# Performance work log

Hardware: AMD Instinct MI355X
Metric: run time of the kernel (lower is better)

Reference implementation:

```python
import jax, jax.numpy as jnp
import numpy as np

N = 100000
E = 1600000
F_IN = 128
F_HID = 64


def setup_inputs() -> dict:
    key = jax.random.key(0)
    ks = jax.random.split(key, 8)
    x = jax.random.normal(ks[0], (N, F_IN), dtype=jnp.float32)
    edge_index = jax.random.randint(ks[1], (2, E), 0, N, dtype=jnp.int64)
    # GCNConv params (PyG default: weight, then bias added after aggregation)
    s1 = 1.0 / np.sqrt(F_IN)
    s2 = 1.0 / np.sqrt(F_HID)
    W1 = jax.random.uniform(ks[2], (F_IN, F_HID), jnp.float32, -s1, s1)
    b1 = jnp.zeros((F_HID,), jnp.float32)
    W2 = jax.random.uniform(ks[3], (F_HID, F_HID), jnp.float32, -s2, s2)
    b2 = jnp.zeros((F_HID,), jnp.float32)
    # Linear(hidden, 1) for predict_link
    Wout = jax.random.uniform(ks[4], (F_HID, 1), jnp.float32, -s2, s2)
    bout = jax.random.uniform(ks[5], (1,), jnp.float32, -s2, s2)
    return {"x": x, "edge_index": edge_index, "W1": W1, "b1": b1,
            "W2": W2, "b2": b2, "Wout": Wout, "bout": bout}


def _gcn_conv(x, row, col, W, b):
    # x: [N, Fin]; row/col: [E'] (self-loops already appended)
    h = x @ W                                              # [N, Fout]
    deg = jax.ops.segment_sum(jnp.ones_like(col, dtype=h.dtype), col,
                              num_segments=N)              # [N]
    dinv = jnp.where(deg > 0, jax.lax.rsqrt(jnp.maximum(deg, 1e-12)), 0.0)
    norm = dinv[row] * dinv[col]                           # [E']
    msg = h[row] * norm[:, None]                           # [E', Fout]
    out = jax.ops.segment_sum(msg, col, num_segments=N)    # [N, Fout]
    return out + b


def reference(x, edge_index, W1, b1, W2, b2, Wout, bout):
    row0, col0 = edge_index[0], edge_index[1]
    # add self-loops (GCNConv default)
    loop = jnp.arange(N, dtype=edge_index.dtype)
    row = jnp.concatenate([row0, loop])
    col = jnp.concatenate([col0, loop])

    h = jax.nn.relu(_gcn_conv(x, row, col, W1, b1))   # dropout p=0.0 (eval)
    h = jax.nn.relu(_gcn_conv(h, row, col, W2, b2))

    # predict_link on the original (no-self-loop) edges
    edge_features = h[row0] * h[col0]                 # [E, F_HID]
    return edge_features @ Wout + bout                # [E, 1]
```

## Files before the change

kernel.cpp:

```cpp
#include <hip/hip_runtime.h>

#define NN 100000
#define EE 1600000
#define FIN 128
#define FHID 64

#define BSH 7
#define NB  ((NN + 127) / 128)
#define CAP 3072
#define BINB NB
#define BIN_EPT 8

typedef union { _Float16 h[4]; uint2 u; } H4;
typedef union { _Float16 h[8]; uint4 u; } H8;
typedef union { _Float16 h[16]; uint4 u[2]; } H16;

__global__ void k_zero_int(int* __restrict__ p, int n) {
    int i = blockIdx.x * blockDim.x + threadIdx.x;
    if (i < n) p[i] = 0;
}

#define XPAD 129

__global__ __launch_bounds__(256) void k_fused(const int* __restrict__ row,
                                               const int* __restrict__ col,
                                               int* __restrict__ bcnt,
                                               unsigned long long* __restrict__ rec,
                                               const float* __restrict__ x,
                                               const float* __restrict__ W1,
                                               uint4* __restrict__ hs16) {
    __shared__ float smem[64 * XPAD];
    int tid = threadIdx.x;
    if (blockIdx.x < BINB) {
        int* hist = (int*)smem;
        int* base = hist + NB;
        for (int i = tid; i < NB; i += 256) hist[i] = 0;
        __syncthreads();
        int e0 = blockIdx.x * (256 * BIN_EPT);
        int b[BIN_EPT];
        int rnk[BIN_EPT];
        unsigned long long pk[BIN_EPT];
#pragma unroll
        for (int j = 0; j < BIN_EPT; ++j) {
            int e = e0 + j * 256 + tid;
            b[j] = -1;
            if (e < EE) {
                int c = col[e];
                int r = row[e];
                b[j] = c >> BSH;
                pk[j] = ((unsigned long long)(unsigned)c << 38) |
                        ((unsigned long long)(unsigned)r << 21) |
                        (unsigned long long)(unsigned)e;
                rnk[j] = atomicAdd(&hist[b[j]], 1);
            }
        }
        __syncthreads();
        for (int i = tid; i < NB; i += 256) {
            int h = hist[i];
            base[i] = h ? atomicAdd(&bcnt[i], h) : 0;
        }
        __syncthreads();
#pragma unroll
        for (int j = 0; j < BIN_EPT; ++j) {
            if (b[j] >= 0) {
                int p = base[b[j]] + rnk[j];
                if (p < CAP) rec[(size_t)b[j] * CAP + p] = pk[j];
            }
        }
    } else {
        int n0 = (blockIdx.x - BINB) * 64;
        const float4* x4 = reinterpret_cast<const float4*>(x);
#pragma unroll
        for (int i = 0; i < 8; ++i) {
            int idx = i * 256 + tid;
            int rw = idx >> 5;
            int k4 = idx & 31;
            float4 v = {0.f, 0.f, 0.f, 0.f};
            if (n0 + rw < NN) v = x4[(size_t)(n0 + rw) * 32 + k4];
            float* p = &smem[rw * XPAD + k4];
            p[0] = v.x; p[32] = v.y; p[64] = v.z; p[96] = v.w;
        }
        __syncthreads();
        int wv = __builtin_amdgcn_readfirstlane(tid >> 6);
        int lane = tid & 63;
        float acc[16];
#pragma unroll
        for (int c = 0; c < 16; ++c) acc[c] = 0.f;
        const float* Wb = W1 + wv * 16;
        const float* xrow = &smem[lane * XPAD];
#pragma unroll 8
        for (int k = 0; k < FIN; ++k) {
            float xk = xrow[((k & 3) << 5) | (k >> 2)];
            const float* wr = Wb + k * FHID;
#pragma unroll
            for (int c = 0; c < 16; ++c) acc[c] = fmaf(xk, wr[c], acc[c]);
        }
        int node = n0 + lane;
        if (node < NN) {
            H16 pk2;
#pragma unroll
            for (int c = 0; c < 16; ++c) pk2.h[c] = (_Float16)acc[c];
            hs16[(size_t)node * 8 + wv * 2] = pk2.u[0];
            hs16[(size_t)node * 8 + wv * 2 + 1] = pk2.u[1];
        }
    }
}

__global__ __launch_bounds__(256) void k_csr(const int* __restrict__ bcnt,
                                             const unsigned long long* __restrict__ rec,
                                             int* __restrict__ csr_src,
                                             int* __restrict__ csr_eid,
                                             int* __restrict__ starts,
                                             int* __restrict__ degi,
                                             float* __restrict__ dinv) {
    __shared__ unsigned short rank[CAP];
    __shared__ int nh[128];
    __shared__ int ns[128];
    __shared__ int nsx[128];
    int b = blockIdx.x;
    int tid = threadIdx.x;
    int cnt = bcnt[b];
    if (cnt > CAP) cnt = CAP;
    int gb = b * CAP;
    const unsigned long long* r = rec + (size_t)b * CAP;
    if (tid < 128) nh[tid] = 0;
    __syncthreads();
    for (int i = tid; i < cnt; i += 256) {
        int c = (int)(r[i] >> 38);
        int cl = c - (b << BSH);
        rank[i] = (unsigned short)atomicAdd(&nh[cl], 1);
    }
    __syncthreads();
    if (tid < 128) ns[tid] = nh[tid];
    __syncthreads();
    for (int off = 1; off < 128; off <<= 1) {
        int x = 0;
        if (tid < 128 && tid >= off) x = ns[tid - off];
        __syncthreads();
        if (tid < 128) ns[tid] += x;
        __syncthreads();
    }
    if (tid < 128) {
        int excl = ns[tid] - nh[tid];
        nsx[tid] = excl;
        int n = (b << BSH) + tid;
        if (n < NN) {
            starts[n] = gb + excl;
            degi[n] = nh[tid];
            dinv[n] = rsqrtf((float)(nh[tid] + 1));
        }
    }
    __syncthreads();
    for (int i = tid; i < cnt; i += 256) {
        unsigned long long rv = r[i];
        int c = (int)(rv >> 38);
        int cl = c - (b << BSH);
        int pos = gb + nsx[cl] + (int)rank[i];
        csr_src[pos] = (int)((rv >> 21) & 0x1FFFF);
        csr_eid[pos] = (int)(rv & 0x1FFFFF);
    }
}

#define X2PAD 65
__global__ __launch_bounds__(256) void k_gemm2(const uint2* __restrict__ y1,
                                               const float* __restrict__ W2,
                                               const float* __restrict__ dinv,
                                               uint4* __restrict__ hs16) {
    __shared__ float al[64 * X2PAD];
    int tid = threadIdx.x;
    int n0 = blockIdx.x * 64;
#pragma unroll
    for (int i = 0; i < 4; ++i) {
        int idx = i * 256 + tid;
        int rw = idx >> 4;
        int k4 = idx & 15;
        float4 v = {0.f, 0.f, 0.f, 0.f};
        if (n0 + rw < NN) {
            H4 t;
            t.u = y1[(size_t)(n0 + rw) * 16 + k4];
            v.x = (float)t.h[0]; v.y = (float)t.h[1];
            v.z = (float)t.h[2]; v.w = (float)t.h[3];
        }
        float* p = &al[rw * X2PAD + k4];
        p[0] = v.x; p[16] = v.y; p[32] = v.z; p[48] = v.w;
    }
    __syncthreads();

    int wv = __builtin_amdgcn_readfirstlane(tid >> 6);
    int lane = tid & 63;
    float acc[16];
#pragma unroll
    for (int c = 0; c < 16; ++c) acc[c] = 0.f;
    const float* Wb = W2 + wv * 16;
    const float* arow = &al[lane * X2PAD];
#pragma unroll 8
    for (int k = 0; k < FHID; ++k) {
        float xk = arow[((k & 3) << 4) | (k >> 2)];
        const float* wr = Wb + k * FHID;
#pragma unroll
        for (int c = 0; c < 16; ++c) acc[c] = fmaf(xk, wr[c], acc[c]);
    }

    int node = n0 + lane;
    if (node < NN) {
        float dn = dinv[node];
        H16 pk;
#pragma unroll
        for (int c = 0; c < 16; ++c) pk.h[c] = (_Float16)(acc[c] * dn);
        hs16[(size_t)node * 8 + wv * 2] = pk.u[0];
        hs16[(size_t)node * 8 + wv * 2 + 1] = pk.u[1];
    }
}

template <int SCALED>
__global__ __launch_bounds__(256) void k_gath(const int* __restrict__ starts,
                                              const int* __restrict__ degi,
                                              const int* __restrict__ csr_src,
                                              const float* __restrict__ dinv,
                                              const uint4* __restrict__ hIn,
                                              const float* __restrict__ bias,
                                              uint4* __restrict__ yOut) {
    int wave = threadIdx.x >> 6;
    int lane = threadIdx.x & 63;
    int g = lane >> 3;
    int fl = lane & 7;
    int n = blockIdx.x * 4 + wave;
    if (n >= NN) return;
    int s = starts[n];
    int d = degi[n];
    float a[8];
    H8 pk;
    if (g == 0) {
        pk.u = hIn[(size_t)n * 8 + fl];
        float dm = SCALED ? 1.f : dinv[n];
#pragma unroll
        for (int j = 0; j < 8; ++j) a[j] = (float)pk.h[j] * dm;
    } else {
#pragma unroll
        for (int j = 0; j < 8; ++j) a[j] = 0.f;
    }
    int k = g;
    for (; k + 8 < d; k += 16) {
        int r0 = csr_src[s + k];
        int r1 = csr_src[s + k + 8];
        H8 v0, v1;
        v0.u = hIn[(size_t)r0 * 8 + fl];
        v1.u = hIn[(size_t)r1 * 8 + fl];
        if (SCALED) {
#pragma unroll
            for (int j = 0; j < 8; ++j) a[j] += (float)v0.h[j] + (float)v1.h[j];
        } else {
            float d0 = dinv[r0], d1 = dinv[r1];
#pragma unroll
            for (int j = 0; j < 8; ++j) {
                a[j] = fmaf((float)v0.h[j], d0, a[j]);
                a[j] = fmaf((float)v1.h[j], d1, a[j]);
            }
        }
    }
    if (k < d) {
        int r = csr_src[s + k];
        pk.u = hIn[(size_t)r * 8 + fl];
        float dm = SCALED ? 1.f : dinv[r];
#pragma unroll
        for (int j = 0; j < 8; ++j) a[j] = fmaf((float)pk.h[j], dm, a[j]);
    }
#pragma unroll
    for (int j = 0; j < 8; ++j) {
        a[j] += __shfl_xor(a[j], 8);
        a[j] += __shfl_xor(a[j], 16);
        a[j] += __shfl_xor(a[j], 32);
    }
    if (g == 0) {
        float dn = dinv[n];
        float4 b0 = reinterpret_cast<const float4*>(bias)[fl * 2];
        float4 b1 = reinterpret_cast<const float4*>(bias)[fl * 2 + 1];
        H8 o;
        o.h[0] = (_Float16)fmaxf(fmaf(a[0], dn, b0.x), 0.f);
        o.h[1] = (_Float16)fmaxf(fmaf(a[1], dn, b0.y), 0.f);
        o.h[2] = (_Float16)fmaxf(fmaf(a[2], dn, b0.z), 0.f);
        o.h[3] = (_Float16)fmaxf(fmaf(a[3], dn, b0.w), 0.f);
        o.h[4] = (_Float16)fmaxf(fmaf(a[4], dn, b1.x), 0.f);
        o.h[5] = (_Float16)fmaxf(fmaf(a[5], dn, b1.y), 0.f);
        o.h[6] = (_Float16)fmaxf(fmaf(a[6], dn, b1.z), 0.f);
        o.h[7] = (_Float16)fmaxf(fmaf(a[7], dn, b1.w), 0.f);
        yOut[(size_t)n * 8 + fl] = o.u;
    }
}

__global__ __launch_bounds__(256) void k_linkc(const int* __restrict__ starts,
                                               const int* __restrict__ degi,
                                               const int* __restrict__ csr_src,
                                               const int* __restrict__ csr_eid,
                                               const uint4* __restrict__ y16,
                                               const float* __restrict__ Wout,
                                               const float* __restrict__ bout,
                                               float* __restrict__ out) {
    int wave = threadIdx.x >> 6;
    int lane = threadIdx.x & 63;
    int g = lane >> 3;
    int fl = lane & 7;
    int n = blockIdx.x * 4 + wave;
    if (n >= NN) return;
    int d = degi[n];
    if (d == 0) return;
    int s = starts[n];
    H8 yc;
    yc.u = y16[(size_t)n * 8 + fl];
    float4 w0 = reinterpret_cast<const float4*>(Wout)[fl * 2];
    float4 w1 = reinterpret_cast<const float4*>(Wout)[fl * 2 + 1];
    float cw[8] = {(float)yc.h[0] * w0.x, (float)yc.h[1] * w0.y,
                   (float)yc.h[2] * w0.z, (float)yc.h[3] * w0.w,
                   (float)yc.h[4] * w1.x, (float)yc.h[5] * w1.y,
                   (float)yc.h[6] * w1.z, (float)yc.h[7] * w1.w};
    float bout0 = bout[0];
    int k = g;
    for (; k + 8 < d; k += 16) {
        int r0 = csr_src[s + k];
        int r1 = csr_src[s + k + 8];
        int e0 = csr_eid[s + k];
        int e1 = csr_eid[s + k + 8];
        H8 v0, v1;
        v0.u = y16[(size_t)r0 * 8 + fl];
        v1.u = y16[(size_t)r1 * 8 + fl];
        float p0 = 0.f, p1 = 0.f;
#pragma unroll
        for (int j = 0; j < 8; ++j) {
            p0 = fmaf((float)v0.h[j], cw[j], p0);
            p1 = fmaf((float)v1.h[j], cw[j], p1);
        }
        p0 += __shfl_xor(p0, 1); p1 += __shfl_xor(p1, 1);
        p0 += __shfl_xor(p0, 2); p1 += __shfl_xor(p1, 2);
        p0 += __shfl_xor(p0, 4); p1 += __shfl_xor(p1, 4);
        if (fl == 0) {
            out[e0] = p0 + bout0;
            out[e1] = p1 + bout0;
        }
    }
    if (k < d) {
        int r = csr_src[s + k];
        int e = csr_eid[s + k];
        H8 v;
        v.u = y16[(size_t)r * 8 + fl];
        float p = 0.f;
#pragma unroll
        for (int j = 0; j < 8; ++j) p = fmaf((float)v.h[j], cw[j], p);
        p += __shfl_xor(p, 1);
        p += __shfl_xor(p, 2);
        p += __shfl_xor(p, 4);
        if (fl == 0) out[e] = p + bout0;
    }
}

extern "C" void kernel_launch(void* const* d_in, const int* in_sizes, int n_in,
                              void* d_out, int out_size, void* d_ws, size_t ws_size,
                              hipStream_t stream) {
    const float* x    = (const float*)d_in[0];
    const int*   ei   = (const int*)d_in[1];
    const float* W1   = (const float*)d_in[2];
    const float* b1   = (const float*)d_in[3];
    const float* W2   = (const float*)d_in[4];
    const float* b2   = (const float*)d_in[5];
    const float* Wout = (const float*)d_in[6];
    const float* bout = (const float*)d_in[7];
    const int*   row0 = ei;
    const int*   col0 = ei + EE;

    char* ws = (char*)d_ws;
    auto align = [](size_t v) { return (v + 255) / 256 * 256; };
    const size_t nInt = align((size_t)NN * 4);
    float* dinv    = (float*)ws;                 ws += nInt;
    int*   degi    = (int*)ws;                   ws += nInt;
    int*   starts  = (int*)ws;                   ws += nInt;
    int*   bcnt    = (int*)ws;                   ws += align((size_t)NB * 4);
    int*   csr_src = (int*)ws;                   ws += align((size_t)NB * CAP * 4);
    int*   csr_eid = (int*)ws;                   ws += align((size_t)NB * CAP * 4);
    unsigned long long* rec = (unsigned long long*)ws;
    ws += align((size_t)NB * CAP * 8);
    uint4* bufH    = (uint4*)ws;                 ws += align((size_t)NN * FHID * 2);
    uint4* bufY    = (uint4*)ws;                 ws += align((size_t)NN * FHID * 2);
    float* out = (float*)d_out;

    const int nTiles = (NN + 63) / 64;

    k_zero_int<<<(NB + 255) / 256, 256, 0, stream>>>(bcnt, NB);
    k_fused<<<BINB + nTiles, 256, 0, stream>>>(row0, col0, bcnt, rec, x, W1, bufH);
    k_csr<<<NB, 256, 0, stream>>>(bcnt, rec, csr_src, csr_eid, starts, degi, dinv);

    k_gath<0><<<(NN + 3) / 4, 256, 0, stream>>>(starts, degi, csr_src, dinv, bufH, b1, bufY);

    k_gemm2<<<nTiles, 256, 0, stream>>>((const uint2*)bufY, W2, dinv, bufH);
    k_gath<1><<<(NN + 3) / 4, 256, 0, stream>>>(starts, degi, csr_src, dinv, bufH, b2, bufY);

    k_linkc<<<(NN + 3) / 4, 256, 0, stream>>>(starts, degi, csr_src, csr_eid,
                                              bufY, Wout, bout, out);
}
```

Measured before the change: 246.3 us.

## Split fused bin/GEMM1 kernel, prescale GEMM1 by dinv, reuse buffer for records

Breaks the combined binning+GEMM1 kernel into a dedicated 1024-thread binning kernel and a separate GEMM1 launched after CSR build, so GEMM1 can multiply its output by dinv of the source node. Both gather passes then use a plain sum without loading dinv per neighbour, removing a scattered dinv load and FMA per edge in layer one. The edge record buffer now aliases bufH to shrink the workspace. The trade-off is that the GEMM1 work no longer overlaps with binning, and the binning grid shape changes.

Measured after the change: 232.9 us. 5.4% less time.

```diff
diff --git a/kernel.cpp b/kernel.cpp
--- a/kernel.cpp
+++ b/kernel.cpp
@@ -8,8 +8,9 @@
 #define BSH 7
 #define NB  ((NN + 127) / 128)
 #define CAP 3072
-#define BINB NB
+#define BIN_BLOCKS 256
 #define BIN_EPT 8
+#define BIN_EPB (1024 * BIN_EPT)
 
 typedef union { _Float16 h[4]; uint2 u; } H4;
 typedef union { _Float16 h[8]; uint4 u; } H8;
@@ -20,88 +21,44 @@
     if (i < n) p[i] = 0;
 }
 
-#define XPAD 129
-
-__global__ __launch_bounds__(256) void k_fused(const int* __restrict__ row,
-                                               const int* __restrict__ col,
-                                               int* __restrict__ bcnt,
-                                               unsigned long long* __restrict__ rec,
-                                               const float* __restrict__ x,
-                                               const float* __restrict__ W1,
-                                               uint4* __restrict__ hs16) {
-    __shared__ float smem[64 * XPAD];
+__global__ __launch_bounds__(1024) void k_bin(const int* __restrict__ row,
+                                              const int* __restrict__ col,
+                                              int* __restrict__ bcnt,
+                                              unsigned long long* __restrict__ rec) {
+    __shared__ int hist[NB];
+    __shared__ int base[NB];
     int tid = threadIdx.x;
-    if (blockIdx.x < BINB) {
-        int* hist = (int*)smem;
-        int* base = hist + NB;
-        for (int i = tid; i < NB; i += 256) hist[i] = 0;
-        __syncthreads();
-        int e0 = blockIdx.x * (256 * BIN_EPT);
-        int b[BIN_EPT];
-        int rnk[BIN_EPT];
-        unsigned long long pk[BIN_EPT];
-#pragma unroll
-        for (int j = 0; j < BIN_EPT; ++j) {
-            int e = e0 + j * 256 + tid;
-            b[j] = -1;
-            if (e < EE) {
-                int c = col[e];
-                int r = row[e];
-                b[j] = c >> BSH;
-                pk[j] = ((unsigned long long)(unsigned)c << 38) |
-                        ((unsigned long long)(unsigned)r << 21) |
-                        (unsigned long long)(unsigned)e;
-                rnk[j] = atomicAdd(&hist[b[j]], 1);
-            }
-        }
-        __syncthreads();
-        for (int i = tid; i < NB; i += 256) {
-            int h = hist[i];
-            base[i] = h ? atomicAdd(&bcnt[i], h) : 0;
-        }
-        __syncthreads();
-#pragma unroll
-        for (int j = 0; j < BIN_EPT; ++j) {
-            if (b[j] >= 0) {
-                int p = base[b[j]] + rnk[j];
-                if (p < CAP) rec[(size_t)b[j] * CAP + p] = pk[j];
-            }
-        }
-    } else {
-        int n0 = (blockIdx.x - BINB) * 64;
-        const float4* x4 = reinterpret_cast<const float4*>(x);
-#pragma unroll
-        for (int i = 0; i < 8; ++i) {
-            int idx = i * 256 + tid;
-            int rw = idx >> 5;
-            int k4 = idx & 31;
-            float4 v = {0.f, 0.f, 0.f, 0.f};
-            if (n0 + rw < NN) v = x4[(size_t)(n0 + rw) * 32 + k4];
-            float* p = &smem[rw * XPAD + k4];
-            p[0] = v.x; p[32] = v.y; p[64] = v.z; p[96] = v.w;
-        }
-        __syncthreads();
-        int wv = __builtin_amdgcn_readfirstlane(tid >> 6);
-        int lane = tid & 63;
-        float acc[16];
-#pragma unroll
-        for (int c = 0; c < 16; ++c) acc[c] = 0.f;
-        const float* Wb = W1 + wv * 16;
-        const float* xrow = &smem[lane * XPAD];
-#pragma unroll 8
-        for (int k = 0; k < FIN; ++k) {
-            float xk = xrow[((k & 3) << 5) | (k >> 2)];
-            const float* wr = Wb + k * FHID;
-#pragma unroll
-            for (int c = 0; c < 16; ++c) acc[c] = fmaf(xk, wr[c], acc[c]);
-        }
-        int node = n0 + lane;
-        if (node < NN) {
-            H16 pk2;
-#pragma unroll
-            for (int c = 0; c < 16; ++c) pk2.h[c] = (_Float16)acc[c];
-            hs16[(size_t)node * 8 + wv * 2] = pk2.u[0];
-            hs16[(size_t)node * 8 + wv * 2 + 1] = pk2.u[1];
+    for (int i = tid; i < NB; i += 1024) hist[i] = 0;
+    __syncthreads();
+    int e0 = blockIdx.x * BIN_EPB;
+    int b[BIN_EPT];
+    int rnk[BIN_EPT];
+    unsigned long long pk[BIN_EPT];
+#pragma unroll
+    for (int j = 0; j < BIN_EPT; ++j) {
+        int e = e0 + j * 1024 + tid;
+        b[j] = -1;
+        if (e < EE) {
+            int c = col[e];
+            int r = row[e];
+            b[j] = c >> BSH;
+            pk[j] = ((unsigned long long)(unsigned)c << 38) |
+                    ((unsigned long long)(unsigned)r << 21) |
+                    (unsigned long long)(unsigned)e;
+            rnk[j] = atomicAdd(&hist[b[j]], 1);
+        }
+    }
+    __syncthreads();
+    for (int i = tid; i < NB; i += 1024) {
+        int h = hist[i];
+        base[i] = h ? atomicAdd(&bcnt[i], h) : 0;
+    }
+    __syncthreads();
+#pragma unroll
+    for (int j = 0; j < BIN_EPT; ++j) {
+        if (b[j] >= 0) {
+            int p = base[b[j]] + rnk[j];
+            if (p < CAP) rec[(size_t)b[j] * CAP + p] = pk[j];
         }
     }
 }
@@ -161,6 +118,53 @@
     }
 }
 
+#define XPAD 129
+__global__ __launch_bounds__(256) void k_gemm1(const float* __restrict__ x,
+                                               const float* __restrict__ W1,
+                                               const float* __restrict__ dinv,
+                                               uint4* __restrict__ hs16) {
+    __shared__ float xl[64 * XPAD];
+    int tid = threadIdx.x;
+    int n0 = blockIdx.x * 64;
+    const float4* x4 = reinterpret_cast<const float4*>(x);
+#pragma unroll
+    for (int i = 0; i < 8; ++i) {
+        int idx = i * 256 + tid;
+        int row = idx >> 5;
+        int k4 = idx & 31;
+        float4 v = {0.f, 0.f, 0.f, 0.f};
+        if (n0 + row < NN) v = x4[(size_t)(n0 + row) * 32 + k4];
+        float* p = &xl[row * XPAD + k4];
+        p[0] = v.x; p[32] = v.y; p[64] = v.z; p[96] = v.w;
+    }
+    __syncthreads();
+
+    int wv = __builtin_amdgcn_readfirstlane(tid >> 6);
+    int lane = tid & 63;
+    float acc[16];
+#pragma unroll
+    for (int c = 0; c < 16; ++c) acc[c] = 0.f;
+    const float* Wb = W1 + wv * 16;
+    const float* xrow = &xl[lane * XPAD];
+#pragma unroll 8
+    for (int k = 0; k < FIN; ++k) {
+        float xk = xrow[((k & 3) << 5) | (k >> 2)];
+        const float* wr = Wb + k * FHID;
+#pragma unroll
+        for (int c = 0; c < 16; ++c) acc[c] = fmaf(xk, wr[c], acc[c]);
+    }
+
+    int node = n0 + lane;
+    if (node < NN) {
+        float dn = dinv[node];
+        H16 pk;
+#pragma unroll
+        for (int c = 0; c < 16; ++c) pk.h[c] = (_Float16)(acc[c] * dn);
+        hs16[(size_t)node * 8 + wv * 2] = pk.u[0];
+        hs16[(size_t)node * 8 + wv * 2 + 1] = pk.u[1];
+    }
+}
+
 #define X2PAD 65
 __global__ __launch_bounds__(256) void k_gemm2(const uint2* __restrict__ y1,
                                                const float* __restrict__ W2,
@@ -212,7 +216,6 @@
     }
 }
 
-template <int SCALED>
 __global__ __launch_bounds__(256) void k_gath(const int* __restrict__ starts,
                                               const int* __restrict__ degi,
                                               const int* __restrict__ csr_src,
@@ -232,9 +235,8 @@
     H8 pk;
     if (g == 0) {
         pk.u = hIn[(size_t)n * 8 + fl];
-        float dm = SCALED ? 1.f : dinv[n];
-#pragma unroll
-        for (int j = 0; j < 8; ++j) a[j] = (float)pk.h[j] * dm;
+#pragma unroll
+        for (int j = 0; j < 8; ++j) a[j] = (float)pk.h[j];
     } else {
 #pragma unroll
         for (int j = 0; j < 8; ++j) a[j] = 0.f;
@@ -246,24 +248,14 @@
         H8 v0, v1;
         v0.u = hIn[(size_t)r0 * 8 + fl];
         v1.u = hIn[(size_t)r1 * 8 + fl];
-        if (SCALED) {
-#pragma unroll
-            for (int j = 0; j < 8; ++j) a[j] += (float)v0.h[j] + (float)v1.h[j];
-        } else {
-            float d0 = dinv[r0], d1 = dinv[r1];
-#pragma unroll
-            for (int j = 0; j < 8; ++j) {
-                a[j] = fmaf((float)v0.h[j], d0, a[j]);
-                a[j] = fmaf((float)v1.h[j], d1, a[j]);
-            }
-        }
+#pragma unroll
+        for (int j = 0; j < 8; ++j) a[j] += (float)v0.h[j] + (float)v1.h[j];
     }
     if (k < d) {
         int r = csr_src[s + k];
         pk.u = hIn[(size_t)r * 8 + fl];
-        float dm = SCALED ? 1.f : dinv[r];
-#pragma unroll
-        for (int j = 0; j < 8; ++j) a[j] = fmaf((float)pk.h[j], dm, a[j]);
+#pragma unroll
+        for (int j = 0; j < 8; ++j) a[j] += (float)pk.h[j];
     }
 #pragma unroll
     for (int j = 0; j < 8; ++j) {
@@ -375,22 +367,22 @@
     int*   bcnt    = (int*)ws;                   ws += align((size_t)NB * 4);
     int*   csr_src = (int*)ws;                   ws += align((size_t)NB * CAP * 4);
     int*   csr_eid = (int*)ws;                   ws += align((size_t)NB * CAP * 4);
-    unsigned long long* rec = (unsigned long long*)ws;
-    ws += align((size_t)NB * CAP * 8);
     uint4* bufH    = (uint4*)ws;                 ws += align((size_t)NN * FHID * 2);
     uint4* bufY    = (uint4*)ws;                 ws += align((size_t)NN * FHID * 2);
+    unsigned long long* rec = (unsigned long long*)bufH;
     float* out = (float*)d_out;
 
     const int nTiles = (NN + 63) / 64;
 
     k_zero_int<<<(NB + 255) / 256, 256, 0, stream>>>(bcnt, NB);
-    k_fused<<<BINB + nTiles, 256, 0, stream>>>(row0, col0, bcnt, rec, x, W1, bufH);
+    k_bin<<<BIN_BLOCKS, 1024, 0, stream>>>(row0, col0, bcnt, rec);
     k_csr<<<NB, 256, 0, stream>>>(bcnt, rec, csr_src, csr_eid, starts, degi, dinv);
 
-    k_gath<0><<<(NN + 3) / 4, 256, 0, stream>>>(starts, degi, csr_src, dinv, bufH, b1, bufY);
+    k_gemm1<<<nTiles, 256, 0, stream>>>(x, W1, dinv, bufH);
+    k_gath<<<(NN + 3) / 4, 256, 0, stream>>>(starts, degi, csr_src, dinv, bufH, b1, bufY);
 
     k_gemm2<<<nTiles, 256, 0, stream>>>((const uint2*)bufY, W2, dinv, bufH);
-    k_gath<1><<<(NN + 3) / 4, 256, 0, stream>>>(starts, degi, csr_src, dinv, bufH, b2, bufY);
+    k_gath<<<(NN + 3) / 4, 256, 0, stream>>>(starts, degi, csr_src, dinv, bufH, b2, bufY);
 
     k_linkc<<<(NN + 3) / 4, 256, 0, stream>>>(starts, degi, csr_src, csr_eid,
                                               bufY, Wout, bout, out);
```
